# Kernel optimization log

Measured on AMD Instinct MI355X. Metric: run time of the kernel, lower is better.

## Reference

```python
import jax, jax.numpy as jnp
import numpy as np

N_PAPER = 100000
N_LABEL = 128
E_CITES = 1600000
E_IS = 100000
F_IN = 128
HID = 128
EMB = 64


def _seg_sum(data, ids, n):
    return jax.ops.segment_sum(data, ids, num_segments=n)


def gcn_conv(x, src, dst, W, b, n):
    # PyG GCNConv: out = D^-1/2 (A+I) D^-1/2 (x W) + b
    h = x @ W
    deg = _seg_sum(jnp.ones(src.shape[0], h.dtype), dst, n) + 1.0  # +1 self loop
    dinv = jax.lax.rsqrt(deg)
    norm = dinv[src] * dinv[dst]                      # [E]
    out = _seg_sum(h[src] * norm[:, None], dst, n)    # neighbor messages
    out = out + (dinv * dinv)[:, None] * h            # self-loop term
    return out + b


def graph_conv(x_src, x_dst, src, dst, W_rel, b_rel, W_root, n_dst):
    # PyG GraphConv: out = lin_rel(sum_j x_j) + lin_root(x_i)
    agg = _seg_sum(x_src[src], dst, n_dst)
    return agg @ W_rel + b_rel + x_dst @ W_root


def hetero_layer(xp, xl, cs, cd, iss, isd, p):
    # outputs onto 'paper' from cites (GCN) and rev_is (GraphConv label->paper): mean of 2
    o_cites = gcn_conv(xp, cs, cd, p['gcn_W'], p['gcn_b'], N_PAPER)
    o_rev = graph_conv(xl, xp, isd, iss, p['rev_relW'], p['rev_relb'], p['rev_rootW'], N_PAPER)
    o_paper = 0.5 * (o_cites + o_rev)
    # output onto 'label' from is (GraphConv paper->label): single conv, mean is identity
    o_label = graph_conv(xp, xl, iss, isd, p['is_relW'], p['is_relb'], p['is_rootW'], N_LABEL)
    return o_paper, o_label


def _init_params(key, d_in, d_out, pfx):
    ks = jax.random.split(key, 8)
    s = 1.0 / np.sqrt(d_in)
    return {
        'gcn_W': jax.random.normal(ks[0], (d_in, d_out), jnp.float32) * s,
        'gcn_b': jnp.zeros((d_out,), jnp.float32),
        'is_relW': jax.random.normal(ks[1], (d_in, d_out), jnp.float32) * s,
        'is_relb': jnp.zeros((d_out,), jnp.float32),
        'is_rootW': jax.random.normal(ks[2], (d_in, d_out), jnp.float32) * s,
        'rev_relW': jax.random.normal(ks[3], (d_in, d_out), jnp.float32) * s,
        'rev_relb': jnp.zeros((d_out,), jnp.float32),
        'rev_rootW': jax.random.normal(ks[4], (d_in, d_out), jnp.float32) * s,
    }


def setup_inputs() -> dict:
    key = jax.random.key(0)
    ks = jax.random.split(key, 10)
    inp = {
        'x_paper': jax.random.normal(ks[0], (N_PAPER, F_IN), jnp.float32),
        'x_label': jax.random.normal(ks[1], (N_LABEL, F_IN), jnp.float32),
        'cites_src': jax.random.randint(ks[2], (E_CITES,), 0, N_PAPER, jnp.int32),
        'cites_dst': jax.random.randint(ks[3], (E_CITES,), 0, N_PAPER, jnp.int32),
        'is_src': jax.random.randint(ks[4], (E_IS,), 0, N_PAPER, jnp.int32),
        'is_dst': jax.random.randint(ks[5], (E_IS,), 0, N_LABEL, jnp.int32),
    }
    p1 = _init_params(ks[6], F_IN, HID, 'l1')
    p2 = _init_params(ks[7], HID, EMB, 'l2')
    for k, v in p1.items():
        inp['l1_' + k] = v
    for k, v in p2.items():
        inp['l2_' + k] = v
    return inp


def reference(x_paper, x_label, cites_src, cites_dst, is_src, is_dst,
              l1_gcn_W, l1_gcn_b, l1_is_relW, l1_is_relb, l1_is_rootW,
              l1_rev_relW, l1_rev_relb, l1_rev_rootW,
              l2_gcn_W, l2_gcn_b, l2_is_relW, l2_is_relb, l2_is_rootW,
              l2_rev_relW, l2_rev_relb, l2_rev_rootW):
    p1 = dict(gcn_W=l1_gcn_W, gcn_b=l1_gcn_b, is_relW=l1_is_relW, is_relb=l1_is_relb,
              is_rootW=l1_is_rootW, rev_relW=l1_rev_relW, rev_relb=l1_rev_relb, rev_rootW=l1_rev_rootW)
    p2 = dict(gcn_W=l2_gcn_W, gcn_b=l2_gcn_b, is_relW=l2_is_relW, is_relb=l2_is_relb,
              is_rootW=l2_is_rootW, rev_relW=l2_rev_relW, rev_relb=l2_rev_relb, rev_rootW=l2_rev_rootW)
    hp, hl = hetero_layer(x_paper, x_label, cites_src, cites_dst, is_src, is_dst, p1)
    hp, hl = jax.nn.relu(hp), jax.nn.relu(hl)
    zp, zl = hetero_layer(hp, hl, cites_src, cites_dst, is_src, is_dst, p2)
    return zp, zl
```

## Files before the change

### kernel.cpp

```cpp
#include <hip/hip_runtime.h>
#include <hip/hip_bf16.h>

#define N_PAPER 100000
#define N_LABEL 128
#define E_CITES 1600000
#define E_IS    100000
#define NBKT    98
#define A2_CHUNK 2048
#define LSPLIT  8
#define CAPC    24576
#define CAPR    2048
#define CAPL    8192

typedef __bf16 bf16x8 __attribute__((ext_vector_type(8)));
typedef float  f32x4  __attribute__((ext_vector_type(4)));
typedef float  f32x2  __attribute__((ext_vector_type(2)));

static __device__ __forceinline__ float bf_lo(unsigned u) {
    union { unsigned u; float f; } v; v.u = u << 16; return v.f;
}
static __device__ __forceinline__ float bf_hi(unsigned u) {
    union { unsigned u; float f; } v; v.u = u & 0xffff0000u; return v.f;
}
static __device__ __forceinline__ unsigned pk_bf(float a, float b) {
    __hip_bfloat16 x = __float2bfloat16(a), y = __float2bfloat16(b);
    unsigned short ux = *(unsigned short*)&x, uy = *(unsigned short*)&y;
    return (unsigned)ux | ((unsigned)uy << 16);
}
static __device__ __forceinline__ unsigned char enc_fp8(float v) {
    return (unsigned char)(__builtin_amdgcn_cvt_pk_fp8_f32(v, v, 0, false) & 0xFF);
}
static __device__ __forceinline__ void dec4(unsigned u, float* o) {
    f32x2 a = __builtin_amdgcn_cvt_pk_f32_fp8((int)u, false);
    f32x2 b = __builtin_amdgcn_cvt_pk_f32_fp8((int)u, true);
    o[0] = a[0]; o[1] = a[1]; o[2] = b[0]; o[3] = b[1];
}

#define NSC ((E_CITES + A2_CHUNK - 1) / A2_CHUNK)
#define NSI ((E_IS + A2_CHUNK - 1) / A2_CHUNK)
__global__ __launch_bounds__(256) void fused_scatter(
    const int* __restrict__ cd, const int* __restrict__ cs,
    const int* __restrict__ iss, const int* __restrict__ isd,
    int* __restrict__ bcur_c, unsigned* __restrict__ ebuf_c,
    int* __restrict__ bcur_r, unsigned* __restrict__ ebuf_r,
    int* __restrict__ bcur_l, unsigned* __restrict__ ebuf_l)
{
    __shared__ int sk[A2_CHUNK], sv[A2_CHUNK];
    __shared__ int h[128], base[128], cur[128];
    int b = blockIdx.x, t = threadIdx.x;
    const int* key; const int* val; int E, shift, b0, cap; int* bcur; unsigned* ebuf;
    if (b < NSC)            { key = cd;  val = cs;  E = E_CITES; bcur = bcur_c; ebuf = ebuf_c; shift = 10; cap = CAPC; b0 = b; }
    else if (b < NSC + NSI) { key = iss; val = isd; E = E_IS;    bcur = bcur_r; ebuf = ebuf_r; shift = 10; cap = CAPR; b0 = b - NSC; }
    else                    { key = isd; val = iss; E = E_IS;    bcur = bcur_l; ebuf = ebuf_l; shift = 0;  cap = CAPL; b0 = b - NSC - NSI; }
    int e0 = b0 * A2_CHUNK;
    int n = min(A2_CHUNK, E - e0);
    for (int i = t; i < 128; i += 256) h[i] = 0;
    __syncthreads();
    for (int i = t; i < n; i += 256) {
        int k = key[e0 + i], v = val[e0 + i];
        sk[i] = k; sv[i] = v;
        atomicAdd(&h[k >> shift], 1);
    }
    __syncthreads();
    for (int i = t; i < 128; i += 256) { base[i] = atomicAdd(&bcur[i], h[i]); cur[i] = 0; }
    __syncthreads();
    for (int i = t; i < n; i += 256) {
        int bb = sk[i] >> shift;
        int p = base[bb] + atomicAdd(&cur[bb], 1);
        ebuf[(size_t)bb * cap + p] = ((unsigned)(sk[i] & 1023) << 17) | (unsigned)sv[i];
    }
}

__global__ __launch_bounds__(1024) void fused_csr(
    const unsigned* __restrict__ ebuf_c, const int* __restrict__ bcnt_c,
    int2* __restrict__ rp2_c, int* __restrict__ col_c, float* __restrict__ dinv,
    const unsigned* __restrict__ ebuf_r, const int* __restrict__ bcnt_r,
    int2* __restrict__ rp2_r, int* __restrict__ col_r)
{
    __shared__ int hist[1024];
    __shared__ int sc[1024];
    int bb = blockIdx.x, t = threadIdx.x;
    const unsigned* ebuf; const int* bcnt; int2* rp2; int* col; float* dv; int b, cap;
    if (bb < NBKT) { ebuf = ebuf_c; bcnt = bcnt_c; rp2 = rp2_c; col = col_c; dv = dinv; b = bb; cap = CAPC; }
    else           { ebuf = ebuf_r; bcnt = bcnt_r; rp2 = rp2_r; col = col_r; dv = nullptr; b = bb - NBKT; cap = CAPR; }
    size_t s = (size_t)b * cap;
    int n = bcnt[b];
    hist[t] = 0;
    __syncthreads();
    for (int i = t; i < n; i += 1024)
        atomicAdd(&hist[ebuf[s + i] >> 17], 1);
    __syncthreads();
    int v = hist[t];
    sc[t] = v;
    __syncthreads();
    for (int off = 1; off < 1024; off <<= 1) {
        int u = (t >= off) ? sc[t - off] : 0;
        __syncthreads();
        sc[t] += u;
        __syncthreads();
    }
    int excl = sc[t] - v;
    int node = b * 1024 + t;
    if (node < N_PAPER) {
        rp2[node] = make_int2((int)(s + excl), (int)(s + excl + v));
        if (dv) dv[node] = rsqrtf((float)v + 1.0f);
    }
    __syncthreads();
    hist[t] = (int)(s + excl);
    __syncthreads();
    for (int i = t; i < n; i += 1024) {
        unsigned u = ebuf[s + i];
        int p = atomicAdd(&hist[u >> 17], 1);
        col[p] = (int)(u & 0x1FFFFu);
    }
}

__global__ __launch_bounds__(256) void fused_prep(
    const float* __restrict__ g1, const float* __restrict__ r1, __hip_bfloat16* __restrict__ Wp1,
    const float* __restrict__ g2, const float* __restrict__ r2, __hip_bfloat16* __restrict__ Wp2,
    const float* __restrict__ xl, const float* __restrict__ W1rev, float* __restrict__ yrev1)
{
    int b = blockIdx.x, t = threadIdx.x;
    if (b < 128 + 64) {
        bool big = (b < 128);
        const float* g = big ? g1 : g2;
        const float* r = big ? r1 : r2;
        __hip_bfloat16* Wp = big ? Wp1 : Wp2;
        int DG = big ? 128 : 64;
        int i = (big ? b : (b - 128)) * 256 + t;
        int j    = i & 7;
        int lane = (i >> 3) & 63;
        int ks   = (i >> 9) & 3;
        int nt   = i >> 11;
        int k = ks * 32 + (lane >> 4) * 8 + j;
        int c = nt * 16 + (lane & 15);
        float v = (c < DG) ? g[k * DG + c] : r[k * DG + (c - DG)];
        Wp[i] = __float2bfloat16(v);
        return;
    }
    __shared__ float xrow[2][128];
    int bb = b - (128 + 64);
    int half = t >> 7, tt = t & 127;
    int l = bb * 2 + half;
    xrow[half][tt] = xl[(size_t)l * 128 + tt];
    __syncthreads();
    float o = 0.f;
    for (int k = 0; k < 128; ++k) o = fmaf(xrow[half][k], W1rev[k * 128 + tt], o);
    yrev1[(size_t)l * 128 + tt] = o;
}

template<int DG, bool AF32>
__global__ __launch_bounds__(512) void gemm_mfma(
    const void* __restrict__ Av, const __hip_bfloat16* __restrict__ Wp,
    const float* __restrict__ dinv,
    unsigned char* __restrict__ Hg, __hip_bfloat16* __restrict__ Hr, int M)
{
    constexpr int NT2 = 2 * DG / 16;
    __shared__ __hip_bfloat16 wlds[NT2 * 2048];
    int tid = threadIdx.x;
    for (int i = tid; i < NT2 * 256; i += 512)
        *(bf16x8*)(wlds + (size_t)i * 8) = *(const bf16x8*)(Wp + (size_t)i * 8);
    __syncthreads();

    int wv = tid >> 6, lane = tid & 63;
    int m0 = blockIdx.x * 128 + wv * 16;
    int row = m0 + (lane & 15);
    int rowc = min(row, M - 1);
    int kg = lane >> 4;

    bf16x8 a[4];
    if constexpr (AF32) {
        const float* ap = (const float*)Av + (size_t)rowc * 128 + kg * 8;
        #pragma unroll
        for (int ks = 0; ks < 4; ++ks) {
            float4 v0 = *(const float4*)(ap + ks * 32);
            float4 v1 = *(const float4*)(ap + ks * 32 + 4);
            bf16x8 f;
            f[0] = (__bf16)v0.x; f[1] = (__bf16)v0.y; f[2] = (__bf16)v0.z; f[3] = (__bf16)v0.w;
            f[4] = (__bf16)v1.x; f[5] = (__bf16)v1.y; f[6] = (__bf16)v1.z; f[7] = (__bf16)v1.w;
            a[ks] = f;
        }
    } else {
        const __hip_bfloat16* ap = (const __hip_bfloat16*)Av + (size_t)rowc * 128 + kg * 8;
        #pragma unroll
        for (int ks = 0; ks < 4; ++ks)
            a[ks] = *(const bf16x8*)(ap + ks * 32);
    }

    f32x4 acc[NT2] = {};
    #pragma unroll
    for (int ks = 0; ks < 4; ++ks) {
        #pragma unroll
        for (int nt = 0; nt < NT2; ++nt) {
            bf16x8 b = *(const bf16x8*)(wlds + ((size_t)(nt * 4 + ks) * 64 + lane) * 8);
            acc[nt] = __builtin_amdgcn_mfma_f32_16x16x32_bf16(a[ks], b, acc[nt], 0, 0, 0);
        }
    }

    int rbase = m0 + (lane >> 4) * 4;
    int c = lane & 15;
    float ds[4];
    #pragma unroll
    for (int r = 0; r < 4; ++r) {
        int rr = rbase + r;
        ds[r] = (rr < M) ? dinv[rr] : 1.f;
    }
    #pragma unroll
    for (int nt = 0; nt < NT2; ++nt) {
        bool isG = (nt < DG / 16);
        if (isG) {
            int cc = nt * 16 + c;
            #pragma unroll
            for (int r = 0; r < 4; ++r) {
                int rr = rbase + r;
                if (rr < M) Hg[(size_t)rr * DG + cc] = enc_fp8(acc[nt][r] * ds[r]);
            }
        } else {
            int cc = (nt - DG / 16) * 16 + c;
            #pragma unroll
            for (int r = 0; r < 4; ++r) {
                int rr = rbase + r;
                if (rr < M) Hr[(size_t)rr * DG + cc] = __float2bfloat16(acc[nt][r]);
            }
        }
    }
}

template<int D, bool RELU, typename OutT>
__global__ __launch_bounds__(256) void paper_assemble(
    const unsigned char* __restrict__ Hg, const __hip_bfloat16* __restrict__ Hr,
    const int2* __restrict__ rp2_c, const int* __restrict__ col_c,
    const float* __restrict__ dinv,
    const int2* __restrict__ rp2_r, const int* __restrict__ col_r,
    const float* __restrict__ yrev,
    const float* __restrict__ gcn_b, const float* __restrict__ rev_relb,
    OutT* __restrict__ out)
{
    constexpr int NB = D / 16;
    constexpr int NP = NB / 2;
    int w = (int)((blockIdx.x * 256 + threadIdx.x) >> 6);
    if (w >= N_PAPER) return;
    int lane = threadIdx.x & 63;
    int grp = lane >> 4, sub = lane & 15;
    unsigned d0 = (unsigned)sub * NB;
    f32x2 a2[NP] = {};
    int2 se = rp2_c[w];
    int s = se.x, e = se.y;
    int j = s + grp;
    for (; j + 4 < e; j += 8) {
        unsigned o0 = (unsigned)col_c[j] * D + d0;
        unsigned o1 = (unsigned)col_c[j + 4] * D + d0;
        if constexpr (NB == 8) {
            uint2 u = *(const uint2*)(Hg + o0);
            uint2 v = *(const uint2*)(Hg + o1);
            a2[0] += __builtin_amdgcn_cvt_pk_f32_fp8((int)u.x, false);
            a2[1] += __builtin_amdgcn_cvt_pk_f32_fp8((int)u.x, true);
            a2[2] += __builtin_amdgcn_cvt_pk_f32_fp8((int)u.y, false);
            a2[3] += __builtin_amdgcn_cvt_pk_f32_fp8((int)u.y, true);
            a2[0] += __builtin_amdgcn_cvt_pk_f32_fp8((int)v.x, false);
            a2[1] += __builtin_amdgcn_cvt_pk_f32_fp8((int)v.x, true);
            a2[2] += __builtin_amdgcn_cvt_pk_f32_fp8((int)v.y, false);
            a2[3] += __builtin_amdgcn_cvt_pk_f32_fp8((int)v.y, true);
        } else {
            unsigned u = *(const unsigned*)(Hg + o0);
            unsigned v = *(const unsigned*)(Hg + o1);
            a2[0] += __builtin_amdgcn_cvt_pk_f32_fp8((int)u, false);
            a2[1] += __builtin_amdgcn_cvt_pk_f32_fp8((int)u, true);
            a2[0] += __builtin_amdgcn_cvt_pk_f32_fp8((int)v, false);
            a2[1] += __builtin_amdgcn_cvt_pk_f32_fp8((int)v, true);
        }
    }
    if (j < e) {
        unsigned o0 = (unsigned)col_c[j] * D + d0;
        if constexpr (NB == 8) {
            uint2 u = *(const uint2*)(Hg + o0);
            a2[0] += __builtin_amdgcn_cvt_pk_f32_fp8((int)u.x, false);
            a2[1] += __builtin_amdgcn_cvt_pk_f32_fp8((int)u.x, true);
            a2[2] += __builtin_amdgcn_cvt_pk_f32_fp8((int)u.y, false);
            a2[3] += __builtin_amdgcn_cvt_pk_f32_fp8((int)u.y, true);
        } else {
            unsigned u = *(const unsigned*)(Hg + o0);
            a2[0] += __builtin_amdgcn_cvt_pk_f32_fp8((int)u, false);
            a2[1] += __builtin_amdgcn_cvt_pk_f32_fp8((int)u, true);
        }
    }
    float acc[NB];
    #pragma unroll
    for (int k = 0; k < NB; ++k) acc[k] = a2[k >> 1][k & 1];
    #pragma unroll
    for (int k = 0; k < NB; ++k) {
        acc[k] += __shfl_xor(acc[k], 16);
        acc[k] += __shfl_xor(acc[k], 32);
    }
    if (grp != 0) return;

    float di = dinv[w];
    float res[NB];
    float sg[NB], sr[NB];
    const unsigned char* hg = Hg + ((unsigned)w * D + d0);
    const __hip_bfloat16* hr = Hr + (size_t)w * D + d0;
    if constexpr (NB == 8) {
        uint2 ug = *(const uint2*)hg;
        dec4(ug.x, sg); dec4(ug.y, sg + 4);
        uint4 ur = *(const uint4*)hr;
        sr[0] = bf_lo(ur.x); sr[1] = bf_hi(ur.x); sr[2] = bf_lo(ur.y); sr[3] = bf_hi(ur.y);
        sr[4] = bf_lo(ur.z); sr[5] = bf_hi(ur.z); sr[6] = bf_lo(ur.w); sr[7] = bf_hi(ur.w);
    } else {
        unsigned ug = *(const unsigned*)hg;
        dec4(ug, sg);
        uint2 ur = *(const uint2*)hr;
        sr[0] = bf_lo(ur.x); sr[1] = bf_hi(ur.x); sr[2] = bf_lo(ur.y); sr[3] = bf_hi(ur.y);
    }
    #pragma unroll
    for (int k = 0; k < NB; ++k)
        res[k] = di * (acc[k] + sg[k]) + sr[k] + gcn_b[d0 + k] + rev_relb[d0 + k];

    int2 se2 = rp2_r[w];
    for (int jj = se2.x; jj < se2.y; ++jj) {
        const float* yr = yrev + (size_t)col_r[jj] * D + d0;
        #pragma unroll
        for (int k = 0; k < NB; ++k) res[k] += yr[k];
    }
    #pragma unroll
    for (int k = 0; k < NB; ++k) {
        res[k] *= 0.5f;
        if (RELU) res[k] = fmaxf(res[k], 0.f);
    }
    if constexpr (sizeof(OutT) == 2) {
        if constexpr (NB == 8) {
            uint4 o = make_uint4(pk_bf(res[0], res[1]), pk_bf(res[2], res[3]),
                                 pk_bf(res[4], res[5]), pk_bf(res[6], res[7]));
            *(uint4*)(out + (size_t)w * D + d0) = o;
        } else {
            uint2 o = make_uint2(pk_bf(res[0], res[1]), pk_bf(res[2], res[3]));
            *(uint2*)(out + (size_t)w * D + d0) = o;
        }
    } else {
        if constexpr (NB == 8) {
            *(float4*)((float*)out + (size_t)w * D + d0) =
                make_float4(res[0], res[1], res[2], res[3]);
            *(float4*)((float*)out + (size_t)w * D + d0 + 4) =
                make_float4(res[4], res[5], res[6], res[7]);
        } else {
            *(float4*)((float*)out + (size_t)w * D + d0) =
                make_float4(res[0], res[1], res[2], res[3]);
        }
    }
}

template<bool AF32>
__global__ __launch_bounds__(128) void label_agg(
    const void* __restrict__ Xv,
    const int* __restrict__ cnt_l, const unsigned* __restrict__ ebuf_l,
    float* __restrict__ partialL)
{
    int l = blockIdx.x, sp = blockIdx.y, t = threadIdx.x;
    int n = cnt_l[l];
    size_t s = (size_t)l * CAPL;
    int per = (n + LSPLIT - 1) / LSPLIT;
    int b = sp * per;
    int en = min(b + per, n);
    float acc = 0.f;
    for (int m = b; m < en; ++m) {
        size_t idx = (size_t)(ebuf_l[s + m] & 0x1FFFFu) * 128 + t;
        if constexpr (AF32) acc += ((const float*)Xv)[idx];
        else                acc += __bfloat162float(((const __hip_bfloat16*)Xv)[idx]);
    }
    partialL[((size_t)l * LSPLIT + sp) * 128 + t] = acc;
}

template<int DOUT, bool RELU, bool YREV2>
__global__ __launch_bounds__(128) void label_finish(
    const float* __restrict__ partialL, const float* __restrict__ Xdst,
    const float* __restrict__ relW, const float* __restrict__ rootW,
    const float* __restrict__ relb, float* __restrict__ out,
    const float* __restrict__ W2rev, float* __restrict__ yrev2)
{
    __shared__ float arow[128];
    __shared__ float xrow[128];
    __shared__ float hrow[128];
    int l = blockIdx.x, t = threadIdx.x;
    float a = 0.f;
    #pragma unroll
    for (int sp = 0; sp < LSPLIT; ++sp)
        a += partialL[((size_t)l * LSPLIT + sp) * 128 + t];
    arow[t] = a;
    xrow[t] = Xdst[(size_t)l * 128 + t];
    __syncthreads();
    float o = 0.f;
    if (t < DOUT) {
        o = relb[t];
        for (int k = 0; k < 128; ++k)
            o = fmaf(arow[k], relW[k * DOUT + t], fmaf(xrow[k], rootW[k * DOUT + t], o));
        if (RELU) o = fmaxf(o, 0.f);
        out[(size_t)l * DOUT + t] = o;
    }
    if constexpr (YREV2) {
        hrow[t] = o;
        __syncthreads();
        if (t < 64) {
            float y = 0.f;
            for (int k = 0; k < 128; ++k)
                y = fmaf(hrow[k], W2rev[k * 64 + t], y);
            yrev2[(size_t)l * 64 + t] = y;
        }
    }
}

extern "C" void kernel_launch(void* const* d_in, const int* in_sizes, int n_in,
                              void* d_out, int out_size, void* d_ws, size_t ws_size,
                              hipStream_t stream)
{
    const float* xp          = (const float*)d_in[0];
    const float* xl          = (const float*)d_in[1];
    const int*   cs          = (const int*)d_in[2];
    const int*   cd          = (const int*)d_in[3];
    const int*   iss         = (const int*)d_in[4];
    const int*   isd         = (const int*)d_in[5];
    const float* l1_gcn_W    = (const float*)d_in[6];
    const float* l1_gcn_b    = (const float*)d_in[7];
    const float* l1_is_relW  = (const float*)d_in[8];
    const float* l1_is_relb  = (const float*)d_in[9];
    const float* l1_is_rootW = (const float*)d_in[10];
    const float* l1_rev_relW = (const float*)d_in[11];
    const float* l1_rev_relb = (const float*)d_in[12];
    const float* l1_rev_rootW= (const float*)d_in[13];
    const float* l2_gcn_W    = (const float*)d_in[14];
    const float* l2_gcn_b    = (const float*)d_in[15];
    const float* l2_is_relW  = (const float*)d_in[16];
    const float* l2_is_relb  = (const float*)d_in[17];
    const float* l2_is_rootW = (const float*)d_in[18];
    const float* l2_rev_relW = (const float*)d_in[19];
    const float* l2_rev_relb = (const float*)d_in[20];
    const float* l2_rev_rootW= (const float*)d_in[21];

    char* ws = (char*)d_ws;
    size_t off = 0;
    auto alloc = [&](size_t bytes) {
        char* p = ws + off;
        off += (bytes + 255) & ~(size_t)255;
        return p;
    };
    __hip_bfloat16* hp1   = (__hip_bfloat16*)alloc((size_t)N_PAPER * 128 * 2);
    unsigned char*  Hg    = (unsigned char*)alloc((size_t)N_PAPER * 128);
    __hip_bfloat16* Hr    = (__hip_bfloat16*)alloc((size_t)N_PAPER * 128 * 2);
    unsigned* ebuf_c = (unsigned*)alloc((size_t)NBKT * CAPC * 4);
    int*      col_c  = (int*)alloc((size_t)NBKT * CAPC * 4);
    unsigned* ebuf_r = (unsigned*)alloc((size_t)NBKT * CAPR * 4);
    int*      col_r  = (int*)alloc((size_t)NBKT * CAPR * 4);
    unsigned* ebuf_l = (unsigned*)alloc((size_t)N_LABEL * CAPL * 4);
    int2*  rp2_c = (int2*)alloc((size_t)N_PAPER * 8);
    int2*  rp2_r = (int2*)alloc((size_t)N_PAPER * 8);
    int*   bcur_c = (int*)alloc((size_t)(NBKT + NBKT + 128) * 4);
    int*   bcur_r = bcur_c + NBKT;
    int*   bcur_l = bcur_r + NBKT;
    float* dinv  = (float*)alloc((size_t)N_PAPER * 4);
    __hip_bfloat16* Wp1 = (__hip_bfloat16*)alloc((size_t)32768 * 2);
    __hip_bfloat16* Wp2 = (__hip_bfloat16*)alloc((size_t)16384 * 2);
    float* yrev1 = (float*)alloc(128 * 128 * 4);
    float* yrev2 = (float*)alloc(128 * 64 * 4);
    float* hl1   = (float*)alloc(128 * 128 * 4);
    float* partialL = (float*)alloc((size_t)N_LABEL * LSPLIT * 128 * 4);

    float* zp = (float*)d_out;
    float* zl = (float*)d_out + (size_t)N_PAPER * 64;

    hipMemsetAsync(bcur_c, 0, (size_t)(NBKT + NBKT + 128) * 4, stream);

    fused_scatter<<<NSC + 2 * NSI, 256, 0, stream>>>(cd, cs, iss, isd,
                                                     bcur_c, ebuf_c, bcur_r, ebuf_r, bcur_l, ebuf_l);
    fused_csr<<<2 * NBKT, 1024, 0, stream>>>(ebuf_c, bcur_c, rp2_c, col_c, dinv,
                                             ebuf_r, bcur_r, rp2_r, col_r);
    fused_prep<<<128 + 64 + 64, 256, 0, stream>>>(
        l1_gcn_W, l1_rev_rootW, Wp1, l2_gcn_W, l2_rev_rootW, Wp2,
        xl, l1_rev_relW, yrev1);

    gemm_mfma<128, true><<<(N_PAPER + 127) / 128, 512, 0, stream>>>(xp, Wp1, dinv, Hg, Hr, N_PAPER);
    paper_assemble<128, true, __hip_bfloat16><<<(N_PAPER + 3) / 4, 256, 0, stream>>>(
        Hg, Hr, rp2_c, col_c, dinv, rp2_r, col_r, yrev1, l1_gcn_b, l1_rev_relb, hp1);
    label_agg<true><<<dim3(N_LABEL, LSPLIT), 128, 0, stream>>>(xp, bcur_l, ebuf_l, partialL);
    label_finish<128, true, true><<<N_LABEL, 128, 0, stream>>>(
        partialL, xl, l1_is_relW, l1_is_rootW, l1_is_relb, hl1, l2_rev_relW, yrev2);

    gemm_mfma<64, false><<<(N_PAPER + 127) / 128, 512, 0, stream>>>(hp1, Wp2, dinv, Hg, Hr, N_PAPER);
    paper_assemble<64, false, float><<<(N_PAPER + 3) / 4, 256, 0, stream>>>(
        Hg, Hr, rp2_c, col_c, dinv, rp2_r, col_r, yrev2, l2_gcn_b, l2_rev_relb, zp);
    label_agg<false><<<dim3(N_LABEL, LSPLIT), 128, 0, stream>>>(hp1, bcur_l, ebuf_l, partialL);
    label_finish<64, false, false><<<N_LABEL, 128, 0, stream>>>(
        partialL, hl1, l2_is_relW, l2_is_rootW, l2_is_relb, zl, nullptr, nullptr);
}
```

Baseline: 305.7 us.

## Fuse prep into scatter, label_agg into assemble, halve CSR buckets

Folds the weight-packing and yrev prep blocks into the scatter kernel, and folds the label aggregation into the paper_assemble launch as extra blocks, which removes several kernel launches. The CSR bucket size drops from 1024 to 512 nodes with 512-thread blocks, giving twice as many buckets and more parallelism in the CSR build. For D=64, paper_assemble now uses 8-lane groups so each lane loads 8 fp8 values, which raises the number of edges processed in parallel per wavefront. The label path also stops packing keys into ebuf_l. The cost is larger kernels with more divergent branches, plus tighter per-bucket capacities.

```diff
diff --git a/kernel.cpp b/kernel.cpp
--- a/kernel.cpp
+++ b/kernel.cpp
@@ -5,12 +5,14 @@
 #define N_LABEL 128
 #define E_CITES 1600000
 #define E_IS    100000
-#define NBKT    98
+#define SH      9
+#define NB2     196
 #define A2_CHUNK 2048
 #define LSPLIT  8
-#define CAPC    24576
-#define CAPR    2048
+#define CAPC    12800
+#define CAPR    1280
 #define CAPL    8192
+#define PA_BLKS 25000
 
 typedef __bf16 bf16x8 __attribute__((ext_vector_type(8)));
 typedef float  f32x4  __attribute__((ext_vector_type(4)));
@@ -38,23 +40,57 @@
 
 #define NSC ((E_CITES + A2_CHUNK - 1) / A2_CHUNK)
 #define NSI ((E_IS + A2_CHUNK - 1) / A2_CHUNK)
+#define PREPB (128 + 64 + 64)
 __global__ __launch_bounds__(256) void fused_scatter(
     const int* __restrict__ cd, const int* __restrict__ cs,
     const int* __restrict__ iss, const int* __restrict__ isd,
     int* __restrict__ bcur_c, unsigned* __restrict__ ebuf_c,
     int* __restrict__ bcur_r, unsigned* __restrict__ ebuf_r,
-    int* __restrict__ bcur_l, unsigned* __restrict__ ebuf_l)
+    int* __restrict__ bcur_l, unsigned* __restrict__ ebuf_l,
+    const float* __restrict__ g1, const float* __restrict__ r1, __hip_bfloat16* __restrict__ Wp1,
+    const float* __restrict__ g2, const float* __restrict__ r2, __hip_bfloat16* __restrict__ Wp2,
+    const float* __restrict__ xl, const float* __restrict__ W1rev, float* __restrict__ yrev1)
 {
     __shared__ int sk[A2_CHUNK], sv[A2_CHUNK];
-    __shared__ int h[128], base[128], cur[128];
+    __shared__ int h[224], base[224], cur[224];
+    __shared__ float xrow[2][128];
     int b = blockIdx.x, t = threadIdx.x;
-    const int* key; const int* val; int E, shift, b0, cap; int* bcur; unsigned* ebuf;
-    if (b < NSC)            { key = cd;  val = cs;  E = E_CITES; bcur = bcur_c; ebuf = ebuf_c; shift = 10; cap = CAPC; b0 = b; }
-    else if (b < NSC + NSI) { key = iss; val = isd; E = E_IS;    bcur = bcur_r; ebuf = ebuf_r; shift = 10; cap = CAPR; b0 = b - NSC; }
-    else                    { key = isd; val = iss; E = E_IS;    bcur = bcur_l; ebuf = ebuf_l; shift = 0;  cap = CAPL; b0 = b - NSC - NSI; }
+    if (b >= NSC + 2 * NSI) {
+        int bp = b - (NSC + 2 * NSI);
+        if (bp < 128 + 64) {
+            bool big = (bp < 128);
+            const float* g = big ? g1 : g2;
+            const float* r = big ? r1 : r2;
+            __hip_bfloat16* Wp = big ? Wp1 : Wp2;
+            int DG = big ? 128 : 64;
+            int i = (big ? bp : (bp - 128)) * 256 + t;
+            int j    = i & 7;
+            int lane = (i >> 3) & 63;
+            int ks   = (i >> 9) & 3;
+            int nt   = i >> 11;
+            int k = ks * 32 + (lane >> 4) * 8 + j;
+            int c = nt * 16 + (lane & 15);
+            float v = (c < DG) ? g[k * DG + c] : r[k * DG + (c - DG)];
+            Wp[i] = __float2bfloat16(v);
+            return;
+        }
+        int bb = bp - (128 + 64);
+        int half = t >> 7, tt = t & 127;
+        int l = bb * 2 + half;
+        xrow[half][tt] = xl[(size_t)l * 128 + tt];
+        __syncthreads();
+        float o = 0.f;
+        for (int k = 0; k < 128; ++k) o = fmaf(xrow[half][k], W1rev[k * 128 + tt], o);
+        yrev1[(size_t)l * 128 + tt] = o;
+        return;
+    }
+    const int* key; const int* val; int E, shift, b0, cap, nb; int* bcur; unsigned* ebuf; bool pack;
+    if (b < NSC)            { key = cd;  val = cs;  E = E_CITES; bcur = bcur_c; ebuf = ebuf_c; shift = SH; cap = CAPC; nb = NB2; b0 = b; pack = true; }
+    else if (b < NSC + NSI) { key = iss; val = isd; E = E_IS;    bcur = bcur_r; ebuf = ebuf_r; shift = SH; cap = CAPR; nb = NB2; b0 = b - NSC; pack = true; }
+    else                    { key = isd; val = iss; E = E_IS;    bcur = bcur_l; ebuf = ebuf_l; shift = 0;  cap = CAPL; nb = 128; b0 = b - NSC - NSI; pack = false; }
     int e0 = b0 * A2_CHUNK;
     int n = min(A2_CHUNK, E - e0);
-    for (int i = t; i < 128; i += 256) h[i] = 0;
+    for (int i = t; i < nb; i += 256) h[i] = 0;
     __syncthreads();
     for (int i = t; i < n; i += 256) {
         int k = key[e0 + i], v = val[e0 + i];
@@ -62,91 +98,62 @@
         atomicAdd(&h[k >> shift], 1);
     }
     __syncthreads();
-    for (int i = t; i < 128; i += 256) { base[i] = atomicAdd(&bcur[i], h[i]); cur[i] = 0; }
+    for (int i = t; i < nb; i += 256) { base[i] = atomicAdd(&bcur[i], h[i]); cur[i] = 0; }
     __syncthreads();
     for (int i = t; i < n; i += 256) {
         int bb = sk[i] >> shift;
         int p = base[bb] + atomicAdd(&cur[bb], 1);
-        ebuf[(size_t)bb * cap + p] = ((unsigned)(sk[i] & 1023) << 17) | (unsigned)sv[i];
-    }
-}
-
-__global__ __launch_bounds__(1024) void fused_csr(
+        unsigned pkv = pack ? (((unsigned)(sk[i] & 511) << 17) | (unsigned)sv[i]) : (unsigned)sv[i];
+        ebuf[(size_t)bb * cap + p] = pkv;
+    }
+}
+
+__global__ __launch_bounds__(512) void fused_csr(
     const unsigned* __restrict__ ebuf_c, const int* __restrict__ bcnt_c,
     int2* __restrict__ rp2_c, int* __restrict__ col_c, float* __restrict__ dinv,
     const unsigned* __restrict__ ebuf_r, const int* __restrict__ bcnt_r,
     int2* __restrict__ rp2_r, int* __restrict__ col_r)
 {
-    __shared__ int hist[1024];
-    __shared__ int sc[1024];
+    __shared__ int hist[512];
+    __shared__ int sc[512];
     int bb = blockIdx.x, t = threadIdx.x;
-    const unsigned* ebuf; const int* bcnt; int2* rp2; int* col; float* dv; int b, cap;
-    if (bb < NBKT) { ebuf = ebuf_c; bcnt = bcnt_c; rp2 = rp2_c; col = col_c; dv = dinv; b = bb; cap = CAPC; }
-    else           { ebuf = ebuf_r; bcnt = bcnt_r; rp2 = rp2_r; col = col_r; dv = nullptr; b = bb - NBKT; cap = CAPR; }
+    bool isC = (bb < NB2);
+    const unsigned* ebuf = isC ? ebuf_c : ebuf_r;
+    const int* bcnt = isC ? bcnt_c : bcnt_r;
+    int2* rp2 = isC ? rp2_c : rp2_r;
+    int* col  = isC ? col_c : col_r;
+    int b = isC ? bb : bb - NB2;
+    int cap = isC ? CAPC : CAPR;
     size_t s = (size_t)b * cap;
     int n = bcnt[b];
     hist[t] = 0;
     __syncthreads();
-    for (int i = t; i < n; i += 1024)
+    for (int i = t; i < n; i += 512)
         atomicAdd(&hist[ebuf[s + i] >> 17], 1);
     __syncthreads();
     int v = hist[t];
     sc[t] = v;
     __syncthreads();
-    for (int off = 1; off < 1024; off <<= 1) {
+    for (int off = 1; off < 512; off <<= 1) {
         int u = (t >= off) ? sc[t - off] : 0;
         __syncthreads();
         sc[t] += u;
         __syncthreads();
     }
     int excl = sc[t] - v;
-    int node = b * 1024 + t;
+    int node = b * 512 + t;
     if (node < N_PAPER) {
         rp2[node] = make_int2((int)(s + excl), (int)(s + excl + v));
-        if (dv) dv[node] = rsqrtf((float)v + 1.0f);
+        if (isC) dinv[node] = rsqrtf((float)v + 1.0f);
     }
     __syncthreads();
     hist[t] = (int)(s + excl);
     __syncthreads();
-    for (int i = t; i < n; i += 1024) {
+    for (int i = t; i < n; i += 512) {
         unsigned u = ebuf[s + i];
         int p = atomicAdd(&hist[u >> 17], 1);
         col[p] = (int)(u & 0x1FFFFu);
     }
-}
-
-__global__ __launch_bounds__(256) void fused_prep(
-    const float* __restrict__ g1, const float* __restrict__ r1, __hip_bfloat16* __restrict__ Wp1,
-    const float* __restrict__ g2, const float* __restrict__ r2, __hip_bfloat16* __restrict__ Wp2,
-    const float* __restrict__ xl, const float* __restrict__ W1rev, float* __restrict__ yrev1)
-{
-    int b = blockIdx.x, t = threadIdx.x;
-    if (b < 128 + 64) {
-        bool big = (b < 128);
-        const float* g = big ? g1 : g2;
-        const float* r = big ? r1 : r2;
-        __hip_bfloat16* Wp = big ? Wp1 : Wp2;
-        int DG = big ? 128 : 64;
-        int i = (big ? b : (b - 128)) * 256 + t;
-        int j    = i & 7;
-        int lane = (i >> 3) & 63;
-        int ks   = (i >> 9) & 3;
-        int nt   = i >> 11;
-        int k = ks * 32 + (lane >> 4) * 8 + j;
-        int c = nt * 16 + (lane & 15);
-        float v = (c < DG) ? g[k * DG + c] : r[k * DG + (c - DG)];
-        Wp[i] = __float2bfloat16(v);
-        return;
-    }
-    __shared__ float xrow[2][128];
-    int bb = b - (128 + 64);
-    int half = t >> 7, tt = t & 127;
-    int l = bb * 2 + half;
-    xrow[half][tt] = xl[(size_t)l * 128 + tt];
-    __syncthreads();
-    float o = 0.f;
-    for (int k = 0; k < 128; ++k) o = fmaf(xrow[half][k], W1rev[k * 128 + tt], o);
-    yrev1[(size_t)l * 128 + tt] = o;
 }
 
 template<int DG, bool AF32>
@@ -226,7 +233,7 @@
     }
 }
 
-template<int D, bool RELU, typename OutT>
+template<int D, bool RELU, typename OutT, bool LAF32>
 __global__ __launch_bounds__(256) void paper_assemble(
     const unsigned char* __restrict__ Hg, const __hip_bfloat16* __restrict__ Hr,
     const int2* __restrict__ rp2_c, const int* __restrict__ col_c,
@@ -234,139 +241,108 @@
     const int2* __restrict__ rp2_r, const int* __restrict__ col_r,
     const float* __restrict__ yrev,
     const float* __restrict__ gcn_b, const float* __restrict__ rev_relb,
-    OutT* __restrict__ out)
-{
-    constexpr int NB = D / 16;
-    constexpr int NP = NB / 2;
-    int w = (int)((blockIdx.x * 256 + threadIdx.x) >> 6);
+    OutT* __restrict__ out,
+    const void* __restrict__ Xl, const int* __restrict__ cnt_l,
+    const unsigned* __restrict__ ebuf_l, float* __restrict__ partialL)
+{
+    constexpr int GL = (D == 128) ? 16 : 8;
+    constexpr int NGRP = 64 / GL;
+    int blk = blockIdx.x;
+    if (blk >= PA_BLKS) {
+        int lb = blk - PA_BLKS;
+        int l = lb >> 2;
+        int t = threadIdx.x;
+        int sp = ((lb & 3) << 1) | (t >> 7);
+        int tt = t & 127;
+        int n = cnt_l[l];
+        size_t s = (size_t)l * CAPL;
+        int per = (n + LSPLIT - 1) / LSPLIT;
+        int b0 = sp * per, en = min(b0 + per, n);
+        float acc = 0.f;
+        for (int m = b0; m < en; ++m) {
+            size_t idx = (size_t)ebuf_l[s + m] * 128 + tt;
+            if constexpr (LAF32) acc += ((const float*)Xl)[idx];
+            else                 acc += __bfloat162float(((const __hip_bfloat16*)Xl)[idx]);
+        }
+        partialL[((size_t)l * LSPLIT + sp) * 128 + tt] = acc;
+        return;
+    }
+    int w = blk * 4 + ((int)threadIdx.x >> 6);
     if (w >= N_PAPER) return;
     int lane = threadIdx.x & 63;
-    int grp = lane >> 4, sub = lane & 15;
-    unsigned d0 = (unsigned)sub * NB;
-    f32x2 a2[NP] = {};
+    int grp = lane / GL, sub = lane % GL;
+    unsigned d0 = (unsigned)sub * 8;
+    f32x2 a2[4] = {};
     int2 se = rp2_c[w];
-    int s = se.x, e = se.y;
-    int j = s + grp;
-    for (; j + 4 < e; j += 8) {
+    int e = se.y;
+    int j = se.x + grp;
+    for (; j + NGRP < e; j += 2 * NGRP) {
         unsigned o0 = (unsigned)col_c[j] * D + d0;
-        unsigned o1 = (unsigned)col_c[j + 4] * D + d0;
-        if constexpr (NB == 8) {
-            uint2 u = *(const uint2*)(Hg + o0);
-            uint2 v = *(const uint2*)(Hg + o1);
-            a2[0] += __builtin_amdgcn_cvt_pk_f32_fp8((int)u.x, false);
-            a2[1] += __builtin_amdgcn_cvt_pk_f32_fp8((int)u.x, true);
-            a2[2] += __builtin_amdgcn_cvt_pk_f32_fp8((int)u.y, false);
-            a2[3] += __builtin_amdgcn_cvt_pk_f32_fp8((int)u.y, true);
-            a2[0] += __builtin_amdgcn_cvt_pk_f32_fp8((int)v.x, false);
-            a2[1] += __builtin_amdgcn_cvt_pk_f32_fp8((int)v.x, true);
-            a2[2] += __builtin_amdgcn_cvt_pk_f32_fp8((int)v.y, false);
-            a2[3] += __builtin_amdgcn_cvt_pk_f32_fp8((int)v.y, true);
-        } else {
-            unsigned u = *(const unsigned*)(Hg + o0);
-            unsigned v = *(const unsigned*)(Hg + o1);
-            a2[0] += __builtin_amdgcn_cvt_pk_f32_fp8((int)u, false);
-            a2[1] += __builtin_amdgcn_cvt_pk_f32_fp8((int)u, true);
-            a2[0] += __builtin_amdgcn_cvt_pk_f32_fp8((int)v, false);
-            a2[1] += __builtin_amdgcn_cvt_pk_f32_fp8((int)v, true);
-        }
+        unsigned o1 = (unsigned)col_c[j + NGRP] * D + d0;
+        uint2 u = *(const uint2*)(Hg + o0);
+        uint2 v = *(const uint2*)(Hg + o1);
+        a2[0] += __builtin_amdgcn_cvt_pk_f32_fp8((int)u.x, false);
+        a2[1] += __builtin_amdgcn_cvt_pk_f32_fp8((int)u.x, true);
+        a2[2] += __builtin_amdgcn_cvt_pk_f32_fp8((int)u.y, false);
+        a2[3] += __builtin_amdgcn_cvt_pk_f32_fp8((int)u.y, true);
+        a2[0] += __builtin_amdgcn_cvt_pk_f32_fp8((int)v.x, false);
+        a2[1] += __builtin_amdgcn_cvt_pk_f32_fp8((int)v.x, true);
+        a2[2] += __builtin_amdgcn_cvt_pk_f32_fp8((int)v.y, false);
+        a2[3] += __builtin_amdgcn_cvt_pk_f32_fp8((int)v.y, true);
     }
     if (j < e) {
         unsigned o0 = (unsigned)col_c[j] * D + d0;
-        if constexpr (NB == 8) {
-            uint2 u = *(const uint2*)(Hg + o0);
-            a2[0] += __builtin_amdgcn_cvt_pk_f32_fp8((int)u.x, false);
-            a2[1] += __builtin_amdgcn_cvt_pk_f32_fp8((int)u.x, true);
-            a2[2] += __builtin_amdgcn_cvt_pk_f32_fp8((int)u.y, false);
-            a2[3] += __builtin_amdgcn_cvt_pk_f32_fp8((int)u.y, true);
-        } else {
-            unsigned u = *(const unsigned*)(Hg + o0);
-            a2[0] += __builtin_amdgcn_cvt_pk_f32_fp8((int)u, false);
-            a2[1] += __builtin_amdgcn_cvt_pk_f32_fp8((int)u, true);
-        }
-    }
-    float acc[NB];
-    #pragma unroll
-    for (int k = 0; k < NB; ++k) acc[k] = a2[k >> 1][k & 1];
-    #pragma unroll
-    for (int k = 0; k < NB; ++k) {
-        acc[k] += __shfl_xor(acc[k], 16);
-        acc[k] += __shfl_xor(acc[k], 32);
+        uint2 u = *(const uint2*)(Hg + o0);
+        a2[0] += __builtin_amdgcn_cvt_pk_f32_fp8((int)u.x, false);
+        a2[1] += __builtin_amdgcn_cvt_pk_f32_fp8((int)u.x, true);
+        a2[2] += __builtin_amdgcn_cvt_pk_f32_fp8((int)u.y, false);
+        a2[3] += __builtin_amdgcn_cvt_pk_f32_fp8((int)u.y, true);
+    }
+    float acc[8];
+    #pragma unroll
+    for (int k = 0; k < 8; ++k) acc[k] = a2[k >> 1][k & 1];
+    #pragma unroll
+    for (int k = 0; k < 8; ++k) {
+        #pragma unroll
+        for (int off = GL; off < 64; off <<= 1)
+            acc[k] += __shfl_xor(acc[k], off);
     }
     if (grp != 0) return;
 
     float di = dinv[w];
-    float res[NB];
-    float sg[NB], sr[NB];
+    float res[8], sg[8], sr[8];
     const unsigned char* hg = Hg + ((unsigned)w * D + d0);
     const __hip_bfloat16* hr = Hr + (size_t)w * D + d0;
-    if constexpr (NB == 8) {
-        uint2 ug = *(const uint2*)hg;
-        dec4(ug.x, sg); dec4(ug.y, sg + 4);
-        uint4 ur = *(const uint4*)hr;
-        sr[0] = bf_lo(ur.x); sr[1] = bf_hi(ur.x); sr[2] = bf_lo(ur.y); sr[3] = bf_hi(ur.y);
-        sr[4] = bf_lo(ur.z); sr[5] = bf_hi(ur.z); sr[6] = bf_lo(ur.w); sr[7] = bf_hi(ur.w);
-    } else {
-        unsigned ug = *(const unsigned*)hg;
-        dec4(ug, sg);
-        uint2 ur = *(const uint2*)hr;
-        sr[0] = bf_lo(ur.x); sr[1] = bf_hi(ur.x); sr[2] = bf_lo(ur.y); sr[3] = bf_hi(ur.y);
-    }
-    #pragma unroll
-    for (int k = 0; k < NB; ++k)
+    uint2 ug = *(const uint2*)hg;
+    dec4(ug.x, sg); dec4(ug.y, sg + 4);
+    uint4 ur = *(const uint4*)hr;
+    sr[0] = bf_lo(ur.x); sr[1] = bf_hi(ur.x); sr[2] = bf_lo(ur.y); sr[3] = bf_hi(ur.y);
+    sr[4] = bf_lo(ur.z); sr[5] = bf_hi(ur.z); sr[6] = bf_lo(ur.w); sr[7] = bf_hi(ur.w);
+    #pragma unroll
+    for (int k = 0; k < 8; ++k)
         res[k] = di * (acc[k] + sg[k]) + sr[k] + gcn_b[d0 + k] + rev_relb[d0 + k];
 
     int2 se2 = rp2_r[w];
     for (int jj = se2.x; jj < se2.y; ++jj) {
         const float* yr = yrev + (size_t)col_r[jj] * D + d0;
         #pragma unroll
-        for (int k = 0; k < NB; ++k) res[k] += yr[k];
-    }
-    #pragma unroll
-    for (int k = 0; k < NB; ++k) {
+        for (int k = 0; k < 8; ++k) res[k] += yr[k];
+    }
+    #pragma unroll
+    for (int k = 0; k < 8; ++k) {
         res[k] *= 0.5f;
         if (RELU) res[k] = fmaxf(res[k], 0.f);
     }
     if constexpr (sizeof(OutT) == 2) {
-        if constexpr (NB == 8) {
-            uint4 o = make_uint4(pk_bf(res[0], res[1]), pk_bf(res[2], res[3]),
-                                 pk_bf(res[4], res[5]), pk_bf(res[6], res[7]));
-            *(uint4*)(out + (size_t)w * D + d0) = o;
-        } else {
-            uint2 o = make_uint2(pk_bf(res[0], res[1]), pk_bf(res[2], res[3]));
-            *(uint2*)(out + (size_t)w * D + d0) = o;
-        }
+        uint4 o = make_uint4(pk_bf(res[0], res[1]), pk_bf(res[2], res[3]),
+                             pk_bf(res[4], res[5]), pk_bf(res[6], res[7]));
+        *(uint4*)(out + (size_t)w * D + d0) = o;
     } else {
-        if constexpr (NB == 8) {
-            *(float4*)((float*)out + (size_t)w * D + d0) =
-                make_float4(res[0], res[1], res[2], res[3]);
-            *(float4*)((float*)out + (size_t)w * D + d0 + 4) =
-                make_float4(res[4], res[5], res[6], res[7]);
-        } else {
-            *(float4*)((float*)out + (size_t)w * D + d0) =
-                make_float4(res[0], res[1], res[2], res[3]);
-        }
-    }
-}
-
-template<bool AF32>
-__global__ __launch_bounds__(128) void label_agg(
-    const void* __restrict__ Xv,
-    const int* __restrict__ cnt_l, const unsigned* __restrict__ ebuf_l,
-    float* __restrict__ partialL)
-{
-    int l = blockIdx.x, sp = blockIdx.y, t = threadIdx.x;
-    int n = cnt_l[l];
-    size_t s = (size_t)l * CAPL;
-    int per = (n + LSPLIT - 1) / LSPLIT;
-    int b = sp * per;
-    int en = min(b + per, n);
-    float acc = 0.f;
-    for (int m = b; m < en; ++m) {
-        size_t idx = (size_t)(ebuf_l[s + m] & 0x1FFFFu) * 128 + t;
-        if constexpr (AF32) acc += ((const float*)Xv)[idx];
-        else                acc += __bfloat162float(((const __hip_bfloat16*)Xv)[idx]);
-    }
-    partialL[((size_t)l * LSPLIT + sp) * 128 + t] = acc;
+        *(float4*)((float*)out + (size_t)w * D + d0) =
+            make_float4(res[0], res[1], res[2], res[3]);
+        *(float4*)((float*)out + (size_t)w * D + d0 + 4) =
+            make_float4(res[4], res[5], res[6], res[7]);
+    }
 }
 
 template<int DOUT, bool RELU, bool YREV2>
@@ -444,16 +420,16 @@
     __hip_bfloat16* hp1   = (__hip_bfloat16*)alloc((size_t)N_PAPER * 128 * 2);
     unsigned char*  Hg    = (unsigned char*)alloc((size_t)N_PAPER * 128);
     __hip_bfloat16* Hr    = (__hip_bfloat16*)alloc((size_t)N_PAPER * 128 * 2);
-    unsigned* ebuf_c = (unsigned*)alloc((size_t)NBKT * CAPC * 4);
-    int*      col_c  = (int*)alloc((size_t)NBKT * CAPC * 4);
-    unsigned* ebuf_r = (unsigned*)alloc((size_t)NBKT * CAPR * 4);
-    int*      col_r  = (int*)alloc((size_t)NBKT * CAPR * 4);
+    unsigned* ebuf_c = (unsigned*)alloc((size_t)NB2 * CAPC * 4);
+    int*      col_c  = (int*)alloc((size_t)NB2 * CAPC * 4);
+    unsigned* ebuf_r = (unsigned*)alloc((size_t)NB2 * CAPR * 4);
+    int*      col_r  = (int*)alloc((size_t)NB2 * CAPR * 4);
     unsigned* ebuf_l = (unsigned*)alloc((size_t)N_LABEL * CAPL * 4);
     int2*  rp2_c = (int2*)alloc((size_t)N_PAPER * 8);
     int2*  rp2_r = (int2*)alloc((size_t)N_PAPER * 8);
-    int*   bcur_c = (int*)alloc((size_t)(NBKT + NBKT + 128) * 4);
-    int*   bcur_r = bcur_c + NBKT;
-    int*   bcur_l = bcur_r + NBKT;
+    int*   bcur_c = (int*)alloc((size_t)(NB2 + NB2 + 128) * 4);
+    int*   bcur_r = bcur_c + NB2;
+    int*   bcur_l = bcur_r + NB2;
     float* dinv  = (float*)alloc((size_t)N_PAPER * 4);
     __hip_bfloat16* Wp1 = (__hip_bfloat16*)alloc((size_t)32768 * 2);
     __hip_bfloat16* Wp2 = (__hip_bfloat16*)alloc((size_t)16384 * 2);
@@ -465,27 +441,26 @@
     float* zp = (float*)d_out;
     float* zl = (float*)d_out + (size_t)N_PAPER * 64;
 
-    hipMemsetAsync(bcur_c, 0, (size_t)(NBKT + NBKT + 128) * 4, stream);
-
-    fused_scatter<<<NSC + 2 * NSI, 256, 0, stream>>>(cd, cs, iss, isd,
-                                                     bcur_c, ebuf_c, bcur_r, ebuf_r, bcur_l, ebuf_l);
-    fused_csr<<<2 * NBKT, 1024, 0, stream>>>(ebuf_c, bcur_c, rp2_c, col_c, dinv,
-                                             ebuf_r, bcur_r, rp2_r, col_r);
-    fused_prep<<<128 + 64 + 64, 256, 0, stream>>>(
+    hipMemsetAsync(bcur_c, 0, (size_t)(NB2 + NB2 + 128) * 4, stream);
+
+    fused_scatter<<<NSC + 2 * NSI + PREPB, 256, 0, stream>>>(
+        cd, cs, iss, isd, bcur_c, ebuf_c, bcur_r, ebuf_r, bcur_l, ebuf_l,
         l1_gcn_W, l1_rev_rootW, Wp1, l2_gcn_W, l2_rev_rootW, Wp2,
         xl, l1_rev_relW, yrev1);
+    fused_csr<<<2 * NB2, 512, 0, stream>>>(ebuf_c, bcur_c, rp2_c, col_c, dinv,
+                                           ebuf_r, bcur_r, rp2_r, col_r);
 
     gemm_mfma<128, true><<<(N_PAPER + 127) / 128, 512, 0, stream>>>(xp, Wp1, dinv, Hg, Hr, N_PAPER);
-    paper_assemble<128, true, __hip_bfloat16><<<(N_PAPER + 3) / 4, 256, 0, stream>>>(
-        Hg, Hr, rp2_c, col_c, dinv, rp2_r, col_r, yrev1, l1_gcn_b, l1_rev_relb, hp1);
-    label_agg<true><<<dim3(N_LABEL, LSPLIT), 128, 0, stream>>>(xp, bcur_l, ebuf_l, partialL);
+    paper_assemble<128, true, __hip_bfloat16, true><<<PA_BLKS + 512, 256, 0, stream>>>(
+        Hg, Hr, rp2_c, col_c, dinv, rp2_r, col_r, yrev1, l1_gcn_b, l1_rev_relb, hp1,
+        xp, bcur_l, ebuf_l, partialL);
     label_finish<128, true, true><<<N_LABEL, 128, 0, stream>>>(
         partialL, xl, l1_is_relW, l1_is_rootW, l1_is_relb, hl1, l2_rev_relW, yrev2);
 
     gemm_mfma<64, false><<<(N_PAPER + 127) / 128, 512, 0, stream>>>(hp1, Wp2, dinv, Hg, Hr, N_PAPER);
-    paper_assemble<64, false, float><<<(N_PAPER + 3) / 4, 256, 0, stream>>>(
-        Hg, Hr, rp2_c, col_c, dinv, rp2_r, col_r, yrev2, l2_gcn_b, l2_rev_relb, zp);
-    label_agg<false><<<dim3(N_LABEL, LSPLIT), 128, 0, stream>>>(hp1, bcur_l, ebuf_l, partialL);
+    paper_assemble<64, false, float, false><<<PA_BLKS + 512, 256, 0, stream>>>(
+        Hg, Hr, rp2_c, col_c, dinv, rp2_r, col_r, yrev2, l2_gcn_b, l2_rev_relb, zp,
+        hp1, bcur_l, ebuf_l, partialL);
     label_finish<64, false, false><<<N_LABEL, 128, 0, stream>>>(
         partialL, hl1, l2_is_relW, l2_is_rootW, l2_is_relb, zl, nullptr, nullptr);
 }
```

After: 335.8 us. +9.9%, slower.
